# Kernel tuning notes

Measured on AMD Instinct MI355X. Metric: run time of the kernel, lower is better.

## Reference

```python
import jax, jax.numpy as jnp
import numpy as np

RADIUS = 0.25
NUM_NEIGHBORS = 32
POS_DIM = 24
STEM_C = 64
PATCH_C = 256
LN_EPS = 1e-5


def query_ball_point(radius, nsample, xyz, new_xyz):
    # xyz: [B,N,3], new_xyz: [B,S,3] -> idx [B,S,nsample] (PointNet++ ball query)
    N = xyz.shape[1]
    sqr = (jnp.sum(new_xyz ** 2, -1)[:, :, None]
           + jnp.sum(xyz ** 2, -1)[:, None, :]
           - 2.0 * jnp.einsum('bsd,bnd->bsn', new_xyz, xyz))  # [B,S,N]
    idx = jnp.broadcast_to(jnp.arange(N, dtype=jnp.int32), sqr.shape)
    idx = jnp.where(sqr > radius * radius, N, idx)
    idx = jnp.sort(idx, axis=-1)[..., :nsample]  # first nsample in-ball (by index order)
    first = idx[..., :1]
    idx = jnp.where(idx == N, first, idx)  # pad empty slots with first neighbor
    return idx


def index_points(points, idx):
    # points [B,N,C], idx [B,S,K] -> [B,S,K,C]
    return jax.vmap(lambda p, i: p[i])(points, idx)


def rel_pos_encoding(rel_xyz, dim=POS_DIM):
    # sinusoidal Fourier encoding of 3D offsets: 3 coords * 2 (sin,cos) * dim//6 freqs
    nf = dim // 6
    freqs = 2.0 ** jnp.arange(nf, dtype=rel_xyz.dtype)
    ang = rel_xyz[..., None] * freqs  # [...,3,nf]
    enc = jnp.concatenate([jnp.sin(ang), jnp.cos(ang)], axis=-1)  # [...,3,2nf]
    return enc.reshape(rel_xyz.shape[:-1] + (dim,))


def point_mlp(x, W, b, gamma, beta, activate):
    h = jnp.einsum('...i,io->...o', x, W) + b
    mu = jnp.mean(h, -1, keepdims=True)
    var = jnp.mean((h - mu) ** 2, -1, keepdims=True)
    h = (h - mu) * jax.lax.rsqrt(var + LN_EPS) * gamma + beta
    return jax.nn.gelu(h, approximate=False) if activate else h


def setup_inputs() -> dict:
    key = jax.random.key(0)
    ks = jax.random.split(key, 8)
    B, N, S = 8, 16384, 1024
    in_c = STEM_C + 3 + POS_DIM  # 91
    return {
        'xyz': jax.random.uniform(ks[0], (B, N, 3), dtype=jnp.float32),
        'point_feature': jax.random.normal(ks[1], (B, N, STEM_C), dtype=jnp.float32),
        'patch_center': jax.random.uniform(ks[2], (B, S, 3), dtype=jnp.float32),
        'W1': jax.random.normal(ks[3], (in_c, PATCH_C), dtype=jnp.float32) * 0.02,
        'b1': jnp.zeros((PATCH_C,), jnp.float32),
        'g1': jnp.ones((PATCH_C,), jnp.float32),
        'be1': jnp.zeros((PATCH_C,), jnp.float32),
        'W2': jax.random.normal(ks[4], (PATCH_C, PATCH_C), dtype=jnp.float32) * 0.02,
        'b2': jnp.zeros((PATCH_C,), jnp.float32),
        'g2': jnp.ones((PATCH_C,), jnp.float32),
        'be2': jnp.zeros((PATCH_C,), jnp.float32),
    }


def reference(xyz, point_feature, patch_center, W1, b1, g1, be1, W2, b2, g2, be2):
    neighbor_idx = query_ball_point(RADIUS, NUM_NEIGHBORS, xyz, patch_center)  # [B,S,K]
    grouped_xyz = index_points(xyz, neighbor_idx)              # [B,S,K,3]
    grouped_feature = index_points(point_feature, neighbor_idx)  # [B,S,K,C]
    relative_xyz = grouped_xyz - patch_center[:, :, None, :]
    relative_position = rel_pos_encoding(relative_xyz)         # [B,S,K,24]
    grouped_input = jnp.concatenate((grouped_feature, relative_xyz, relative_position), axis=-1)
    h = point_mlp(grouped_input, W1, b1, g1, be1, True)
    h = point_mlp(h, W2, b2, g2, be2, False)
    patch_feature = jnp.max(h, axis=2)                         # max over neighbors -> [B,S,PATCH_C]
    return patch_feature, neighbor_idx
```

## Files before the change

kernel.cpp:

```cpp
#include <hip/hip_runtime.h>
#include <math.h>

#define NPTS 16384
#define KN 32
#define C 256
#define NQ 8192
#define PF_ELEMS (NQ * C)

#define W1P_ELEMS (3 * 16 * 64 * 8)
#define W2P_ELEMS (8 * 16 * 64 * 8)
#define HSTR 264

typedef _Float16 half8 __attribute__((ext_vector_type(8)));
typedef _Float16 half4v __attribute__((ext_vector_type(4)));
typedef _Float16 half2t __attribute__((ext_vector_type(2)));
typedef float f32x4 __attribute__((ext_vector_type(4)));

union H8u { half8 v; half2t h2[4]; };

__device__ __forceinline__ float fdot2f(half2t a, half2t b, float c) {
#if __has_builtin(__builtin_amdgcn_fdot2)
    return __builtin_amdgcn_fdot2(a, b, c, false);
#else
    return fmaf((float)a[1], (float)b[1], fmaf((float)a[0], (float)b[0], c));
#endif
}

__device__ __forceinline__ float gelu_tanh(float x) {
    const float t  = x * x;
    const float p2 = fmaf(t, 0.0713548162726f, 1.59576912161f);
    const float e  = __expf(x * p2);
    return x - x * __builtin_amdgcn_rcpf(e + 1.0f);
}

__device__ __forceinline__ void stat8(const H8u& u, half2t ones, float& s, float& s2) {
    #pragma unroll
    for (int j = 0; j < 4; ++j) {
        s  = fdot2f(u.h2[j], ones, s);
        s2 = fdot2f(u.h2[j], u.h2[j], s2);
    }
}

__device__ __forceinline__ void norm_gelu8(H8u& u, const H8u& g, const H8u& be,
                                           half2t rsh, half2t nmuh) {
    #pragma unroll
    for (int j = 0; j < 4; ++j) {
        const half2t A = g.h2[j] * rsh;
        const half2t B = A * nmuh + be.h2[j];
        const half2t y = u.h2[j] * A + B;
        half2t o;
        o[0] = (_Float16)gelu_tanh((float)y[0]);
        o[1] = (_Float16)gelu_tanh((float)y[1]);
        u.h2[j] = o;
    }
}

__device__ __forceinline__ void norm8(H8u& u, const H8u& g, const H8u& be,
                                      half2t rsh, half2t nmuh) {
    #pragma unroll
    for (int j = 0; j < 4; ++j) {
        const half2t A = g.h2[j] * rsh;
        const half2t B = A * nmuh + be.h2[j];
        u.h2[j] = u.h2[j] * A + B;
    }
}

__global__ void prep_w_kernel(const float* __restrict__ W1,
                              const float* __restrict__ b1,
                              const float* __restrict__ W2,
                              _Float16* __restrict__ wp) {
    const int idx = blockIdx.x * 256 + threadIdx.x;
    if (idx < 96 * 256) {
        const int k = idx >> 8, n = idx & 255;
        const float v = (k < 91) ? W1[k * 256 + n] : ((k == 91) ? b1[n] : 0.0f);
        const int kt = k >> 5, quad = (k >> 3) & 3, j = k & 7;
        const int nt = n >> 4, l15 = n & 15;
        wp[(((kt * 16 + nt) * 64) + quad * 16 + l15) * 8 + j] = (_Float16)v;
    } else {
        const int e = idx - 96 * 256;
        const int k = e >> 8, n = e & 255;
        const int kt = k >> 5, quad = (k >> 3) & 3, j = k & 7;
        const int nt = n >> 4, l15 = n & 15;
        wp[W1P_ELEMS + (((kt * 16 + nt) * 64) + quad * 16 + l15) * 8 + j] =
            (_Float16)W2[k * 256 + n];
    }
}

__global__ void __launch_bounds__(256, 6)
encoder_fused(const float* __restrict__ xyz,
              const float* __restrict__ pf,
              const float* __restrict__ ctr,
              const float* __restrict__ g1, const float* __restrict__ be1,
              const float* __restrict__ b2, const float* __restrict__ g2,
              const float* __restrict__ be2,
              const _Float16* __restrict__ w1p,
              const _Float16* __restrict__ w2p,
              float* __restrict__ out0,
              float* __restrict__ out1) {
    const int q = blockIdx.x;
    const int b = q >> 10;
    const int t = threadIdx.x;
    const int w = t >> 6;
    const int lane = t & 63;
    const int quad = lane >> 4;
    const int l15  = lane & 15;

    __shared__ __align__(16) unsigned char H16raw[KN * HSTR * 2];
    __shared__ __align__(16) _Float16 lnph[4 * 256];
    __shared__ int nbr[KN];
    __shared__ int wcnt[2][4];

    _Float16 (*H16)[HSTR] = (_Float16(*)[HSTR])H16raw;
    _Float16 (*Xs)[104]   = (_Float16(*)[104])H16raw;
    _Float16* g1h  = lnph;
    _Float16* be1h = lnph + 256;
    _Float16* g2h  = lnph + 512;
    _Float16* be2h = lnph + 768;

    lnph[t]       = (_Float16)g1[t];
    lnph[256 + t] = (_Float16)be1[t];
    lnph[512 + t] = (_Float16)g2[t];
    lnph[768 + t] = (_Float16)be2[t];

    const float* xb = xyz + (size_t)b * NPTS * 3;
    const float cx = ctr[q * 3 + 0];
    const float cy = ctr[q * 3 + 1];
    const float cz = ctr[q * 3 + 2];
    const float sc = __fadd_rn(__fadd_rn(__fmul_rn(cx, cx), __fmul_rn(cy, cy)),
                               __fmul_rn(cz, cz));

    int found = 0;
    int par = 0;
    for (int base = 0; base < NPTS; base += 256) {
        const int n = base + t;
        const float px = xb[n * 3 + 0];
        const float py = xb[n * 3 + 1];
        const float pz = xb[n * 3 + 2];
        const float sp = __fadd_rn(__fadd_rn(__fmul_rn(px, px), __fmul_rn(py, py)),
                                   __fmul_rn(pz, pz));
        const float dt = __fadd_rn(__fadd_rn(__fmul_rn(cx, px), __fmul_rn(cy, py)),
                                   __fmul_rn(cz, pz));
        const float sqr = __fsub_rn(__fadd_rn(sc, sp), __fmul_rn(2.0f, dt));
        const bool inball = (sqr <= 0.0625f);

        const unsigned long long m = __ballot(inball);
        if (lane == 0) wcnt[par][w] = (int)__popcll(m);
        __syncthreads();
        int pre = found;
        if (w > 0) pre += wcnt[par][0];
        if (w > 1) pre += wcnt[par][1];
        if (w > 2) pre += wcnt[par][2];
        const int tot = found + wcnt[par][0] + wcnt[par][1] + wcnt[par][2] + wcnt[par][3];
        const int pos = pre + (int)__popcll(m & ((1ull << lane) - 1ull));
        if (inball && pos < KN) nbr[pos] = n;
        found = tot;
        par ^= 1;
        if (found >= KN) break;
    }
    __syncthreads();
    const int count = (found < KN) ? found : KN;
    const int first = (count > 0) ? nbr[0] : NPTS;

    if (t < KN)
        out1[(size_t)q * KN + t] = (float)((t < count) ? nbr[t] : first);

    {
        const int k  = t >> 3;
        const int tc = t & 7;
        const int nidx = (k < count) ? nbr[k] : first;
        const int n = (nidx < NPTS) ? nidx : NPTS - 1;
        const float rx = xb[n * 3 + 0] - cx;
        const float ry = xb[n * 3 + 1] - cy;
        const float rz = xb[n * 3 + 2] - cz;
        const float* pfr = pf + ((size_t)b * NPTS + n) * 64;

        const float4 f0 = *(const float4*)(pfr + tc * 8);
        const float4 f1 = *(const float4*)(pfr + tc * 8 + 4);
        half8 hv;
        hv[0] = (_Float16)f0.x; hv[1] = (_Float16)f0.y;
        hv[2] = (_Float16)f0.z; hv[3] = (_Float16)f0.w;
        hv[4] = (_Float16)f1.x; hv[5] = (_Float16)f1.y;
        hv[6] = (_Float16)f1.z; hv[7] = (_Float16)f1.w;
        *(half8*)&Xs[k][tc * 8] = hv;

        half4v ov;
        #pragma unroll
        for (int j = 0; j < 4; ++j) {
            const int c = 64 + tc * 4 + j;
            float v;
            if (c < 67) {
                v = (c == 64) ? rx : ((c == 65) ? ry : rz);
            } else if (c < 91) {
                const int jj = c - 67;
                const int d = jj >> 3;
                const int mm = jj & 7;
                const float f = (float)(1 << (mm & 3));
                const float r = (d == 0) ? rx : ((d == 1) ? ry : rz);
                v = (mm < 4) ? __sinf(r * f) : __cosf(r * f);
            } else if (c == 91) {
                v = 1.0f;
            } else {
                v = 0.0f;
            }
            ov[j] = (_Float16)v;
        }
        *(half4v*)&Xs[k][64 + tc * 4] = ov;
    }
    __syncthreads();

    f32x4 acc[2][4];

    #pragma unroll
    for (int mt = 0; mt < 2; ++mt)
        #pragma unroll
        for (int nt = 0; nt < 4; ++nt)
            acc[mt][nt] = (f32x4){0.f, 0.f, 0.f, 0.f};

    #pragma unroll
    for (int kt = 0; kt < 3; ++kt) {
        const half8 x0 = *(const half8*)&Xs[l15][kt * 32 + quad * 8];
        const half8 x1 = *(const half8*)&Xs[16 + l15][kt * 32 + quad * 8];
        #pragma unroll
        for (int nt = 0; nt < 4; ++nt) {
            const half8 wf = *(const half8*)&w1p[((kt * 16 + w * 4 + nt) * 64 + lane) * 8];
            acc[0][nt] = __builtin_amdgcn_mfma_f32_16x16x32_f16(wf, x0, acc[0][nt], 0, 0, 0);
            acc[1][nt] = __builtin_amdgcn_mfma_f32_16x16x32_f16(wf, x1, acc[1][nt], 0, 0, 0);
        }
    }
    __syncthreads();

    #pragma unroll
    for (int nt = 0; nt < 4; ++nt) {
        const int chb = (w * 4 + nt) * 16 + quad * 4;
        #pragma unroll
        for (int mt = 0; mt < 2; ++mt) {
            half4v h;
            #pragma unroll
            for (int r = 0; r < 4; ++r)
                h[r] = (_Float16)acc[mt][nt][r];
            *(half4v*)&H16[mt * 16 + l15][chb] = h;
        }
    }
    __syncthreads();

    const int row = t >> 3;
    const int p   = t & 7;
    _Float16* hrow0 = &H16[row][16 * p];
    _Float16* hrow1 = &H16[row][128 + 16 * p];
    half2t ones;
    ones[0] = (_Float16)1.0f;
    ones[1] = (_Float16)1.0f;

    {
        H8u u0, u1, u2, u3;
        u0.v = *(const half8*)hrow0;
        u1.v = *(const half8*)(hrow0 + 8);
        u2.v = *(const half8*)hrow1;
        u3.v = *(const half8*)(hrow1 + 8);

        float s = 0.0f, s2 = 0.0f;
        stat8(u0, ones, s, s2); stat8(u1, ones, s, s2);
        stat8(u2, ones, s, s2); stat8(u3, ones, s, s2);
        #pragma unroll
        for (int off = 1; off < 8; off <<= 1) {
            s  += __shfl_xor(s, off, 64);
            s2 += __shfl_xor(s2, off, 64);
        }
        const float mu  = s * (1.0f / 256.0f);
        const float var = fmaf(s2, 1.0f / 256.0f, -mu * mu);
        const float rs  = __builtin_amdgcn_rsqf(var + 1e-5f);
        half2t rsh, nmuh;
        rsh[0]  = (_Float16)rs;    rsh[1]  = (_Float16)rs;
        nmuh[0] = (_Float16)(-mu); nmuh[1] = (_Float16)(-mu);

        H8u gA0, gA1, gB0, gB1, bA0, bA1, bB0, bB1;
        gA0.v = *(const half8*)&g1h[16 * p];        bA0.v = *(const half8*)&be1h[16 * p];
        gA1.v = *(const half8*)&g1h[16 * p + 8];    bA1.v = *(const half8*)&be1h[16 * p + 8];
        gB0.v = *(const half8*)&g1h[128 + 16 * p];  bB0.v = *(const half8*)&be1h[128 + 16 * p];
        gB1.v = *(const half8*)&g1h[136 + 16 * p];  bB1.v = *(const half8*)&be1h[136 + 16 * p];

        norm_gelu8(u0, gA0, bA0, rsh, nmuh);
        norm_gelu8(u1, gA1, bA1, rsh, nmuh);
        norm_gelu8(u2, gB0, bB0, rsh, nmuh);
        norm_gelu8(u3, gB1, bB1, rsh, nmuh);

        *(half8*)hrow0       = u0.v;
        *(half8*)(hrow0 + 8) = u1.v;
        *(half8*)hrow1       = u2.v;
        *(half8*)(hrow1 + 8) = u3.v;
    }
    __syncthreads();

    #pragma unroll
    for (int mt = 0; mt < 2; ++mt)
        #pragma unroll
        for (int nt = 0; nt < 4; ++nt)
            acc[mt][nt] = (f32x4){0.f, 0.f, 0.f, 0.f};

    #pragma unroll
    for (int kt = 0; kt < 8; ++kt) {
        const half8 h0 = *(const half8*)&H16[l15][kt * 32 + quad * 8];
        const half8 h1 = *(const half8*)&H16[16 + l15][kt * 32 + quad * 8];
        #pragma unroll
        for (int nt = 0; nt < 4; ++nt) {
            const half8 wf = *(const half8*)&w2p[((kt * 16 + w * 4 + nt) * 64 + lane) * 8];
            acc[0][nt] = __builtin_amdgcn_mfma_f32_16x16x32_f16(wf, h0, acc[0][nt], 0, 0, 0);
            acc[1][nt] = __builtin_amdgcn_mfma_f32_16x16x32_f16(wf, h1, acc[1][nt], 0, 0, 0);
        }
    }
    __syncthreads();

    #pragma unroll
    for (int nt = 0; nt < 4; ++nt) {
        const int chb = (w * 4 + nt) * 16 + quad * 4;
        const f32x4 bv = *(const f32x4*)&b2[chb];
        #pragma unroll
        for (int mt = 0; mt < 2; ++mt) {
            half4v h;
            #pragma unroll
            for (int r = 0; r < 4; ++r)
                h[r] = (_Float16)(acc[mt][nt][r] + bv[r]);
            *(half4v*)&H16[mt * 16 + l15][chb] = h;
        }
    }
    __syncthreads();

    {
        H8u u0, u1, u2, u3;
        u0.v = *(const half8*)hrow0;
        u1.v = *(const half8*)(hrow0 + 8);
        u2.v = *(const half8*)hrow1;
        u3.v = *(const half8*)(hrow1 + 8);

        float s = 0.0f, s2 = 0.0f;
        stat8(u0, ones, s, s2); stat8(u1, ones, s, s2);
        stat8(u2, ones, s, s2); stat8(u3, ones, s, s2);
        #pragma unroll
        for (int off = 1; off < 8; off <<= 1) {
            s  += __shfl_xor(s, off, 64);
            s2 += __shfl_xor(s2, off, 64);
        }
        const float mu  = s * (1.0f / 256.0f);
        const float var = fmaf(s2, 1.0f / 256.0f, -mu * mu);
        const float rs  = __builtin_amdgcn_rsqf(var + 1e-5f);
        half2t rsh, nmuh;
        rsh[0]  = (_Float16)rs;    rsh[1]  = (_Float16)rs;
        nmuh[0] = (_Float16)(-mu); nmuh[1] = (_Float16)(-mu);

        H8u gA0, gA1, gB0, gB1, bA0, bA1, bB0, bB1;
        gA0.v = *(const half8*)&g2h[16 * p];        bA0.v = *(const half8*)&be2h[16 * p];
        gA1.v = *(const half8*)&g2h[16 * p + 8];    bA1.v = *(const half8*)&be2h[16 * p + 8];
        gB0.v = *(const half8*)&g2h[128 + 16 * p];  bB0.v = *(const half8*)&be2h[128 + 16 * p];
        gB1.v = *(const half8*)&g2h[136 + 16 * p];  bB1.v = *(const half8*)&be2h[136 + 16 * p];

        norm8(u0, gA0, bA0, rsh, nmuh);
        norm8(u1, gA1, bA1, rsh, nmuh);
        norm8(u2, gB0, bB0, rsh, nmuh);
        norm8(u3, gB1, bB1, rsh, nmuh);

        *(half8*)hrow0       = u0.v;
        *(half8*)(hrow0 + 8) = u1.v;
        *(half8*)hrow1       = u2.v;
        *(half8*)(hrow1 + 8) = u3.v;
    }
    __syncthreads();

    if (t < 128) {
        const _Float16* Hf = &H16[0][0];
        half2t mx = *(const half2t*)(Hf + 2 * t);
        #pragma unroll
        for (int r = 1; r < KN; ++r) {
            const half2t v = *(const half2t*)(Hf + r * HSTR + 2 * t);
            mx = __builtin_elementwise_max(mx, v);
        }
        float2 o2;
        o2.x = (float)mx[0];
        o2.y = (float)mx[1];
        *(float2*)&out0[(size_t)q * C + 2 * t] = o2;
    }
}

extern "C" void kernel_launch(void* const* d_in, const int* in_sizes, int n_in,
                              void* d_out, int out_size, void* d_ws, size_t ws_size,
                              hipStream_t stream) {
    const float* xyz = (const float*)d_in[0];
    const float* pf  = (const float*)d_in[1];
    const float* ctr = (const float*)d_in[2];
    const float* W1  = (const float*)d_in[3];
    const float* b1  = (const float*)d_in[4];
    const float* g1  = (const float*)d_in[5];
    const float* be1 = (const float*)d_in[6];
    const float* W2  = (const float*)d_in[7];
    const float* b2  = (const float*)d_in[8];
    const float* g2  = (const float*)d_in[9];
    const float* be2 = (const float*)d_in[10];

    float* out = (float*)d_out;
    _Float16* wp = (_Float16*)d_ws;

    prep_w_kernel<<<(96 * 256 + 65536) / 256, 256, 0, stream>>>(W1, b1, W2, wp);
    encoder_fused<<<NQ, 256, 0, stream>>>(xyz, pf, ctr,
                                          g1, be1, b2, g2, be2,
                                          wp, wp + W1P_ELEMS,
                                          out, out + PF_ELEMS);
}
```

Baseline: 191.8 us.

## Precompute float4 xyz with squared norm, separate Xs buffer, cheaper encoding

The prep kernel now also packs each point into a float4 of (x, y, z, |p|^2). The ball-query scan then does one vector load per point and skips recomputing the norm, at the cost of an extra workspace array and a few more prep blocks. Xs gets its own shared buffer instead of aliasing H16, which lets one __syncthreads after the first GEMM go; this raises LDS use and may lower occupancy. The Fourier encoding now uses a single hardware sin with a quarter-period phase shift for cosine, and weight pointers are made wave-uniform via readfirstlane.

```diff
diff --git a/kernel.cpp b/kernel.cpp
--- a/kernel.cpp
+++ b/kernel.cpp
@@ -9,6 +9,7 @@
 
 #define W1P_ELEMS (3 * 16 * 64 * 8)
 #define W2P_ELEMS (8 * 16 * 64 * 8)
+#define WP_ELEMS  (W1P_ELEMS + W2P_ELEMS)
 #define HSTR 264
 
 typedef _Float16 half8 __attribute__((ext_vector_type(8)));
@@ -65,10 +66,12 @@
     }
 }
 
-__global__ void prep_w_kernel(const float* __restrict__ W1,
-                              const float* __restrict__ b1,
-                              const float* __restrict__ W2,
-                              _Float16* __restrict__ wp) {
+__global__ void prep_kernel(const float* __restrict__ W1,
+                            const float* __restrict__ b1,
+                            const float* __restrict__ W2,
+                            const float* __restrict__ xyz,
+                            _Float16* __restrict__ wp,
+                            float4* __restrict__ xyzw) {
     const int idx = blockIdx.x * 256 + threadIdx.x;
     if (idx < 96 * 256) {
         const int k = idx >> 8, n = idx & 255;
@@ -76,18 +79,26 @@
         const int kt = k >> 5, quad = (k >> 3) & 3, j = k & 7;
         const int nt = n >> 4, l15 = n & 15;
         wp[(((kt * 16 + nt) * 64) + quad * 16 + l15) * 8 + j] = (_Float16)v;
-    } else {
+    } else if (idx < WP_ELEMS) {
         const int e = idx - 96 * 256;
         const int k = e >> 8, n = e & 255;
         const int kt = k >> 5, quad = (k >> 3) & 3, j = k & 7;
         const int nt = n >> 4, l15 = n & 15;
         wp[W1P_ELEMS + (((kt * 16 + nt) * 64) + quad * 16 + l15) * 8 + j] =
             (_Float16)W2[k * 256 + n];
+    } else {
+        const int pi = idx - WP_ELEMS;
+        const float px = xyz[pi * 3 + 0];
+        const float py = xyz[pi * 3 + 1];
+        const float pz = xyz[pi * 3 + 2];
+        const float sp = __fadd_rn(__fadd_rn(__fmul_rn(px, px), __fmul_rn(py, py)),
+                                   __fmul_rn(pz, pz));
+        xyzw[pi] = make_float4(px, py, pz, sp);
     }
 }
 
 __global__ void __launch_bounds__(256, 6)
-encoder_fused(const float* __restrict__ xyz,
+encoder_fused(const float4* __restrict__ xyzw,
               const float* __restrict__ pf,
               const float* __restrict__ ctr,
               const float* __restrict__ g1, const float* __restrict__ be1,
@@ -105,13 +116,13 @@
     const int quad = lane >> 4;
     const int l15  = lane & 15;
 
+    __shared__ __align__(16) _Float16 Xs[KN][104];
     __shared__ __align__(16) unsigned char H16raw[KN * HSTR * 2];
     __shared__ __align__(16) _Float16 lnph[4 * 256];
     __shared__ int nbr[KN];
     __shared__ int wcnt[2][4];
 
     _Float16 (*H16)[HSTR] = (_Float16(*)[HSTR])H16raw;
-    _Float16 (*Xs)[104]   = (_Float16(*)[104])H16raw;
     _Float16* g1h  = lnph;
     _Float16* be1h = lnph + 256;
     _Float16* g2h  = lnph + 512;
@@ -122,7 +133,7 @@
     lnph[512 + t] = (_Float16)g2[t];
     lnph[768 + t] = (_Float16)be2[t];
 
-    const float* xb = xyz + (size_t)b * NPTS * 3;
+    const float4* xwb = xyzw + (size_t)b * NPTS;
     const float cx = ctr[q * 3 + 0];
     const float cy = ctr[q * 3 + 1];
     const float cz = ctr[q * 3 + 2];
@@ -133,14 +144,10 @@
     int par = 0;
     for (int base = 0; base < NPTS; base += 256) {
         const int n = base + t;
-        const float px = xb[n * 3 + 0];
-        const float py = xb[n * 3 + 1];
-        const float pz = xb[n * 3 + 2];
-        const float sp = __fadd_rn(__fadd_rn(__fmul_rn(px, px), __fmul_rn(py, py)),
-                                   __fmul_rn(pz, pz));
-        const float dt = __fadd_rn(__fadd_rn(__fmul_rn(cx, px), __fmul_rn(cy, py)),
-                                   __fmul_rn(cz, pz));
-        const float sqr = __fsub_rn(__fadd_rn(sc, sp), __fmul_rn(2.0f, dt));
+        const float4 pw = xwb[n];
+        const float dt = __fadd_rn(__fadd_rn(__fmul_rn(cx, pw.x), __fmul_rn(cy, pw.y)),
+                                   __fmul_rn(cz, pw.z));
+        const float sqr = __fsub_rn(__fadd_rn(sc, pw.w), __fmul_rn(2.0f, dt));
         const bool inball = (sqr <= 0.0625f);
 
         const unsigned long long m = __ballot(inball);
@@ -169,9 +176,10 @@
         const int tc = t & 7;
         const int nidx = (k < count) ? nbr[k] : first;
         const int n = (nidx < NPTS) ? nidx : NPTS - 1;
-        const float rx = xb[n * 3 + 0] - cx;
-        const float ry = xb[n * 3 + 1] - cy;
-        const float rz = xb[n * 3 + 2] - cz;
+        const float4 pw = xwb[n];
+        const float rx = pw.x - cx;
+        const float ry = pw.y - cy;
+        const float rz = pw.z - cz;
         const float* pfr = pf + ((size_t)b * NPTS + n) * 64;
 
         const float4 f0 = *(const float4*)(pfr + tc * 8);
@@ -186,22 +194,20 @@
         half4v ov;
         #pragma unroll
         for (int j = 0; j < 4; ++j) {
-            const int c = 64 + tc * 4 + j;
-            float v;
-            if (c < 67) {
-                v = (c == 64) ? rx : ((c == 65) ? ry : rz);
-            } else if (c < 91) {
-                const int jj = c - 67;
-                const int d = jj >> 3;
-                const int mm = jj & 7;
-                const float f = (float)(1 << (mm & 3));
-                const float r = (d == 0) ? rx : ((d == 1) ? ry : rz);
-                v = (mm < 4) ? __sinf(r * f) : __cosf(r * f);
-            } else if (c == 91) {
-                v = 1.0f;
-            } else {
-                v = 0.0f;
-            }
+            const int cm = tc * 4 + j;
+            const int jj = cm - 3;
+            const int d  = jj >> 3;
+            const int mm = jj & 7;
+            const float rsel = (d == 0) ? rx : ((d == 1) ? ry : rz);
+            const float f2 = __int_as_float(0x3E22F983 + ((mm & 3) << 23));
+            const float arg = fmaf(rsel, f2, (mm >= 4) ? 0.25f : 0.0f);
+#if __has_builtin(__builtin_amdgcn_sinf)
+            const float sv = __builtin_amdgcn_sinf(arg);
+#else
+            const float sv = __sinf(arg * 6.2831853071795864f);
+#endif
+            float v = (cm < 3) ? ((cm == 0) ? rx : ((cm == 1) ? ry : rz)) : sv;
+            v = (cm == 27) ? 1.0f : ((cm > 27) ? 0.0f : v);
             ov[j] = (_Float16)v;
         }
         *(half4v*)&Xs[k][64 + tc * 4] = ov;
@@ -209,6 +215,11 @@
     __syncthreads();
 
     f32x4 acc[2][4];
+
+    const int wu = __builtin_amdgcn_readfirstlane(w);
+    const _Float16* __restrict__ w1w = w1p + (size_t)(wu * 4) * 512;
+    const _Float16* __restrict__ w2w = w2p + (size_t)(wu * 4) * 512;
+    const int lo8 = lane * 8;
 
     #pragma unroll
     for (int mt = 0; mt < 2; ++mt)
@@ -222,12 +233,11 @@
         const half8 x1 = *(const half8*)&Xs[16 + l15][kt * 32 + quad * 8];
         #pragma unroll
         for (int nt = 0; nt < 4; ++nt) {
-            const half8 wf = *(const half8*)&w1p[((kt * 16 + w * 4 + nt) * 64 + lane) * 8];
+            const half8 wf = *(const half8*)(w1w + (kt * 16 + nt) * 512 + lo8);
             acc[0][nt] = __builtin_amdgcn_mfma_f32_16x16x32_f16(wf, x0, acc[0][nt], 0, 0, 0);
             acc[1][nt] = __builtin_amdgcn_mfma_f32_16x16x32_f16(wf, x1, acc[1][nt], 0, 0, 0);
         }
     }
-    __syncthreads();
 
     #pragma unroll
     for (int nt = 0; nt < 4; ++nt) {
@@ -303,7 +313,7 @@
         const half8 h1 = *(const half8*)&H16[16 + l15][kt * 32 + quad * 8];
         #pragma unroll
         for (int nt = 0; nt < 4; ++nt) {
-            const half8 wf = *(const half8*)&w2p[((kt * 16 + w * 4 + nt) * 64 + lane) * 8];
+            const half8 wf = *(const half8*)(w2w + (kt * 16 + nt) * 512 + lo8);
             acc[0][nt] = __builtin_amdgcn_mfma_f32_16x16x32_f16(wf, h0, acc[0][nt], 0, 0, 0);
             acc[1][nt] = __builtin_amdgcn_mfma_f32_16x16x32_f16(wf, h1, acc[1][nt], 0, 0, 0);
         }
@@ -397,9 +407,10 @@
 
     float* out = (float*)d_out;
     _Float16* wp = (_Float16*)d_ws;
-
-    prep_w_kernel<<<(96 * 256 + 65536) / 256, 256, 0, stream>>>(W1, b1, W2, wp);
-    encoder_fused<<<NQ, 256, 0, stream>>>(xyz, pf, ctr,
+    float4* xyzw = (float4*)(wp + WP_ELEMS);
+
+    prep_kernel<<<(WP_ELEMS + NPTS * 8) / 256, 256, 0, stream>>>(W1, b1, W2, xyz, wp, xyzw);
+    encoder_fused<<<NQ, 256, 0, stream>>>(xyzw, pf, ctr,
                                           g1, be1, b2, g2, be2,
                                           wp, wp + W1P_ELEMS,
                                           out, out + PF_ELEMS);
```

Measured after the change: 184.0 us. 1.04x faster.
